# Performance work log

Measured on AMD Instinct MI355X. Metric: run time of the kernel, lower is better.

## Reference

```python
import jax, jax.numpy as jnp
import numpy as np

B, N, D, H, QK, FF, E, K = 32, 400, 128, 8, 16, 512, 8, 2
LOSS_COEF = 1e-2


def layer_norm(x, g, b, eps=1e-5):
    m = x.mean(-1, keepdims=True)
    v = ((x - m) ** 2).mean(-1, keepdims=True)
    return (x - m) / jnp.sqrt(v + eps) * g + b


def cv_sq(x, eps=1e-10):
    return x.var() / (x.mean() ** 2 + eps)


def setup_inputs() -> dict:
    key = jax.random.key(0)
    ks = jax.random.split(key, 10)
    w = lambda i, shape: jax.random.normal(ks[i], shape, jnp.float32) * 0.02
    return {
        "x": jax.random.normal(ks[0], (B, N, D), jnp.float32),
        "Wq": w(1, (D, H * QK)),
        "Wk": w(2, (D, H * QK)),
        "Wv": w(3, (D, H * QK)),
        "Wo": w(4, (H * QK, D)),
        "bo": jnp.zeros((D,), jnp.float32),
        "ln1_g": jnp.ones((D,), jnp.float32),
        "ln1_b": jnp.zeros((D,), jnp.float32),
        "w_gate": w(5, (D, E)),
        "W1": w(6, (E, D, FF)),
        "b1": jnp.zeros((E, FF), jnp.float32),
        "W2": w(7, (E, FF, D)),
        "b2": jnp.zeros((E, D), jnp.float32),
        "ln2_g": jnp.ones((D,), jnp.float32),
        "ln2_b": jnp.zeros((D,), jnp.float32),
    }


def reference(x, Wq, Wk, Wv, Wo, bo, ln1_g, ln1_b, w_gate, W1, b1, W2, b2, ln2_g, ln2_b):
    b, n, d = x.shape
    # multi-head self-attention (no mask in encoder)
    q = (x @ Wq).reshape(b, n, H, QK).transpose(0, 2, 1, 3)  # [b,h,n,qk]
    k = (x @ Wk).reshape(b, n, H, QK).transpose(0, 2, 1, 3)
    v = (x @ Wv).reshape(b, n, H, QK).transpose(0, 2, 1, 3)
    score = jnp.einsum("bhnd,bhmd->bhnm", q, k) / (QK ** 0.5)
    weights = jax.nn.softmax(score, axis=-1)
    out = jnp.einsum("bhnm,bhmd->bhnd", weights, v)
    out_concat = out.transpose(0, 2, 1, 3).reshape(b, n, H * QK)
    mh = out_concat @ Wo + bo
    out1 = layer_norm(x + mh, ln1_g, ln1_b)

    # MoE feed-forward: noisy top-k gating in eval mode (clean logits)
    xf = out1.reshape(-1, d)                       # [T, D]
    T = xf.shape[0]
    logits = xf @ w_gate                           # [T, E]
    top_vals, top_idx = jax.lax.top_k(logits, K)   # [T, K]
    top_gates = jax.nn.softmax(top_vals, axis=-1)
    gates = jnp.zeros((T, E), xf.dtype).at[jnp.arange(T)[:, None], top_idx].set(top_gates)
    # dense per-expert compute, sparse combine (same math as dispatch/combine)
    h = jax.nn.relu(jnp.einsum("td,edf->etf", xf, W1) + b1[:, None, :])  # [E,T,FF]
    y = jnp.einsum("etf,efd->etd", h, W2) + b2[:, None, :]               # [E,T,D]
    moe_out = jnp.einsum("etd,te->td", y, gates).reshape(b, n, d)
    importance = gates.sum(0)
    load = (gates > 0).sum(0).astype(xf.dtype)
    moe_loss = (cv_sq(importance) + cv_sq(load)) * LOSS_COEF

    out3 = layer_norm(out1 + moe_out, ln2_g, ln2_b)
    return (out3, moe_loss)
```

## Files before the change

### kernel.cpp

```cpp
#include <hip/hip_runtime.h>
#include <hip/hip_bf16.h>
#include <math.h>

#define Bb 32
#define Nn 400
#define Dd 128
#define Hh 8
#define QKd 16
#define FFd 512
#define Ee 8
#define Tt (Bb*Nn)
#define KPAD 434
#define PP2 34

typedef __attribute__((ext_vector_type(8))) __bf16 bf16x8;
typedef __attribute__((ext_vector_type(4))) float f32x4;

#if defined(__has_builtin)
#if __has_builtin(__builtin_amdgcn_exp2f)
#define EXP2(x) __builtin_amdgcn_exp2f(x)
#endif
#endif
#ifndef EXP2
#define EXP2(x) __expf((x) * 0.69314718f)
#endif

__device__ __forceinline__ unsigned short f2bfu(float f){
  union { __hip_bfloat16 h; unsigned short u; } v;
  v.h = __float2bfloat16(f);
  return v.u;
}
__device__ __forceinline__ short f2bf(float f){ return (short)f2bfu(f); }
__device__ __forceinline__ unsigned pack2bf(float a, float b){
  return (unsigned)f2bfu(a) | ((unsigned)f2bfu(b) << 16);
}
__device__ __forceinline__ bf16x8 zero_bf16x8(){
  union { uint4 u; bf16x8 b; } z;
  z.u.x = 0u; z.u.y = 0u; z.u.z = 0u; z.u.w = 0u;
  return z.b;
}

__global__ __launch_bounds__(256) void prep_kernel(
    const float* __restrict__ W1, const float* __restrict__ W2, const float* __restrict__ Wo,
    const float* __restrict__ Wq, const float* __restrict__ Wk, const float* __restrict__ Wv,
    short* __restrict__ W1t, short* __restrict__ W2t, short* __restrict__ wo_t,
    short* __restrict__ qkvw, int* __restrict__ gmeta)
{
  const int bid = blockIdx.x;
  if (bid == 0 && threadIdx.x < 24) gmeta[threadIdx.x] = 0;

  const float* in; short* out; int C, tile;
  if (bid < 512)        { int e = bid >> 6;         tile = bid & 63;          in = W1 + e*65536; out = W1t + e*65536; C = 512; }
  else if (bid < 1024)  { int e = (bid - 512) >> 6; tile = (bid - 512) & 63;  in = W2 + e*65536; out = W2t + e*65536; C = 128; }
  else if (bid < 1040)  { tile = bid - 1024; in = Wo; out = wo_t;          C = 128; }
  else if (bid < 1056)  { tile = bid - 1040; in = Wq; out = qkvw;          C = 128; }
  else if (bid < 1072)  { tile = bid - 1056; in = Wk; out = qkvw + 16384;  C = 128; }
  else                  { tile = bid - 1072; in = Wv; out = qkvw + 32768;  C = 128; }
  const int R = (bid < 512) ? 128 : (bid < 1024 ? 512 : 128);

  __shared__ float t32[32][33];
  const int nCt = C >> 5;
  const int c0 = (tile % nCt) << 5;
  const int r0 = (tile / nCt) << 5;
  const int tx = threadIdx.x & 31, ty = threadIdx.x >> 5;
  #pragma unroll
  for (int i = 0; i < 4; ++i)
    t32[ty + 8*i][tx] = in[(size_t)(r0 + ty + 8*i) * C + c0 + tx];
  __syncthreads();
  #pragma unroll
  for (int i = 0; i < 4; ++i)
    out[(size_t)(c0 + ty + 8*i) * R + r0 + tx] = f2bf(t32[tx][ty + 8*i]);
}

__global__ __launch_bounds__(512) void qkv_kernel(const float* __restrict__ x,
    const short* __restrict__ qkvw,
    short* __restrict__ q, short* __restrict__ k, short* __restrict__ v)
{
  __shared__ short xsh[64][136];
  __shared__ short xsl[64][136];
  const int tid = threadIdx.x;
  const int t0 = blockIdx.x * 64;

  #pragma unroll
  for (int it = 0; it < 4; ++it) {
    int lin = it * 512 + tid;
    int r = lin >> 5;
    int c4 = (lin & 31) << 2;
    float4 xv = *(const float4*)&x[(size_t)(t0 + r) * Dd + c4];
    unsigned h01 = pack2bf(xv.x, xv.y);
    unsigned h23 = pack2bf(xv.z, xv.w);
    union { unsigned u; float f; } ua, ub, uc, ud;
    ua.u = h01 << 16; ub.u = h01 & 0xFFFF0000u;
    uc.u = h23 << 16; ud.u = h23 & 0xFFFF0000u;
    unsigned l01 = pack2bf(xv.x - ua.f, xv.y - ub.f);
    unsigned l23 = pack2bf(xv.z - uc.f, xv.w - ud.f);
    uint2 ph; ph.x = h01; ph.y = h23;
    uint2 pl; pl.x = l01; pl.y = l23;
    *(uint2*)&xsh[r][c4] = ph;
    *(uint2*)&xsl[r][c4] = pl;
  }
  __syncthreads();

  const int lane = tid & 63, w = tid >> 6;
  const int l15 = lane & 15, l4 = lane >> 4;

  f32x4 zero4 = {0.f, 0.f, 0.f, 0.f};
  f32x4 acc[3][4];
  #pragma unroll
  for (int ot = 0; ot < 3; ++ot)
    #pragma unroll
    for (int mt = 0; mt < 4; ++mt) acc[ot][mt] = zero4;

  #pragma unroll
  for (int kt = 0; kt < 4; ++kt) {
    bf16x8 bmh[4], bml[4];
    #pragma unroll
    for (int mt = 0; mt < 4; ++mt) {
      bmh[mt] = *(const bf16x8*)&xsh[mt*16 + l15][kt*32 + l4*8];
      bml[mt] = *(const bf16x8*)&xsl[mt*16 + l15][kt*32 + l4*8];
    }
    #pragma unroll
    for (int ot = 0; ot < 3; ++ot) {
      bf16x8 a = *(const bf16x8*)&qkvw[(size_t)(w*48 + ot*16 + l15) * Dd + kt*32 + l4*8];
      #pragma unroll
      for (int mt = 0; mt < 4; ++mt) {
        acc[ot][mt] = __builtin_amdgcn_mfma_f32_16x16x32_bf16(a, bmh[mt], acc[ot][mt], 0, 0, 0);
        acc[ot][mt] = __builtin_amdgcn_mfma_f32_16x16x32_bf16(a, bml[mt], acc[ot][mt], 0, 0, 0);
      }
    }
  }

  #pragma unroll
  for (int ot = 0; ot < 3; ++ot) {
    const int ob = w*48 + ot*16;
    const int sel = ob >> 7;
    const int hz = (ob & 127) >> 4;
    #pragma unroll
    for (int mt = 0; mt < 4; ++mt) {
      int t = t0 + mt*16 + l15;
      int b = t / Nn, n = t - b * Nn;
      size_t bhn = (size_t)(b*Hh + hz) * Nn + n;
      f32x4 a = acc[ot][mt];
      uint2 p;
      if (sel == 0) {
        p.x = pack2bf(a[0]*0.36067376f, a[1]*0.36067376f);
        p.y = pack2bf(a[2]*0.36067376f, a[3]*0.36067376f);
        *(uint2*)&q[bhn*16 + l4*4] = p;
      } else if (sel == 1) {
        p.x = pack2bf(a[0], a[1]);
        p.y = pack2bf(a[2], a[3]);
        *(uint2*)&k[bhn*16 + l4*4] = p;
      } else {
        p.x = pack2bf(a[0], a[1]);
        p.y = pack2bf(a[2], a[3]);
        *(uint2*)&v[bhn*16 + l4*4] = p;
      }
    }
  }
}

__global__ __launch_bounds__(1024) void attn_kernel(const short* __restrict__ q,
    const short* __restrict__ k, const short* __restrict__ v, short* __restrict__ attn_b)
{
  __shared__ short VT[16 * KPAD];
  __shared__ short P[16][4][16 * PP2];
  const int tid = threadIdx.x;
  const int bh = blockIdx.x;

  {
    const unsigned* vg = (const unsigned*)(v + (size_t)bh * 400 * 16);
    #pragma unroll
    for (int it = 0; it < 4; ++it) {
      int lin = it*1024 + tid;
      if (lin < 3200) {
        int key = lin >> 3, dp = lin & 7;
        unsigned pv = vg[key*8 + dp];
        VT[(2*dp)  * KPAD + key] = (short)(pv & 0xffffu);
        VT[(2*dp+1)* KPAD + key] = (short)(pv >> 16);
      }
    }
    if (tid < 256) {
      int d = tid >> 4, key = 400 + (tid & 15);
      VT[d*KPAD + key] = 0;
    }
  }
  __syncthreads();

  const int w = tid >> 6, lane = tid & 63;
  const int l15 = lane & 15, g = lane >> 4;
  const int p = w & 7, hh = w >> 3;
  const int cc0 = hh ? 7 : 0;
  const int cc1 = hh ? 13 : 7;

  f32x4 zero4 = {0.f, 0.f, 0.f, 0.f};
  f32x4 o[4];
  float lsum[4];
  bf16x8 qf[4];
  #pragma unroll
  for (int i = 0; i < 4; ++i) {
    o[i] = zero4; lsum[i] = 0.f;
    int qt = p + 8*i;
    if (qt < 25 && g < 2)
      qf[i] = *(const bf16x8*)&q[((size_t)bh*400 + qt*16 + l15)*16 + 8*g];
    else
      qf[i] = zero_bf16x8();
  }

  for (int cc = cc0; cc < cc1; ++cc) {
    #pragma unroll
    for (int sub = 0; sub < 2; ++sub) {
      const int kt = cc*2 + sub;
      if (kt < 25) {
        bf16x8 kf;
        if (g < 2) kf = *(const bf16x8*)&k[((size_t)bh*400 + kt*16 + l15)*16 + 8*g];
        else       kf = zero_bf16x8();
        #pragma unroll
        for (int i = 0; i < 4; ++i) {
          int qt = p + 8*i;
          if (qt < 25) {
            f32x4 s = __builtin_amdgcn_mfma_f32_16x16x32_bf16(kf, qf[i], zero4, 0, 0, 0);
            float p0 = EXP2(s[0]);
            float p1 = EXP2(s[1]);
            float p2 = EXP2(s[2]);
            float p3 = EXP2(s[3]);
            lsum[i] += (p0 + p1) + (p2 + p3);
            uint2 pk;
            pk.x = pack2bf(p0, p1);
            pk.y = pack2bf(p2, p3);
            *(uint2*)&P[w][i][l15*PP2 + sub*16 + 4*g] = pk;
          }
        }
      } else {
        uint2 z; z.x = 0u; z.y = 0u;
        #pragma unroll
        for (int i = 0; i < 4; ++i) {
          int qt = p + 8*i;
          if (qt < 25) *(uint2*)&P[w][i][l15*PP2 + sub*16 + 4*g] = z;
        }
      }
    }
    bf16x8 vf = *(const bf16x8*)&VT[l15*KPAD + cc*32 + 8*g];
    #pragma unroll
    for (int i = 0; i < 4; ++i) {
      int qt = p + 8*i;
      if (qt < 25) {
        bf16x8 pf = *(const bf16x8*)&P[w][i][l15*PP2 + 8*g];
        o[i] = __builtin_amdgcn_mfma_f32_16x16x32_bf16(vf, pf, o[i], 0, 0, 0);
      }
    }
  }

  #pragma unroll
  for (int i = 0; i < 4; ++i) {
    lsum[i] += __shfl_xor(lsum[i], 16, 64);
    lsum[i] += __shfl_xor(lsum[i], 32, 64);
  }

  __syncthreads();
  float* CB = (float*)&P[0][0][0];
  if (hh == 1) {
    #pragma unroll
    for (int i = 0; i < 4; ++i) {
      int qt = p + 8*i;
      if (qt < 25) {
        int base = (((p*4) + i)*64 + lane)*5;
        CB[base+0] = o[i][0]; CB[base+1] = o[i][1];
        CB[base+2] = o[i][2]; CB[base+3] = o[i][3];
        CB[base+4] = lsum[i];
      }
    }
  }
  __syncthreads();
  if (hh == 0) {
    const int b = bh >> 3, h = bh & 7;
    #pragma unroll
    for (int i = 0; i < 4; ++i) {
      int qt = p + 8*i;
      if (qt < 25) {
        int base = (((p*4) + i)*64 + lane)*5;
        float o0 = o[i][0] + CB[base+0];
        float o1 = o[i][1] + CB[base+1];
        float o2 = o[i][2] + CB[base+2];
        float o3 = o[i][3] + CB[base+3];
        float ls = lsum[i] + CB[base+4];
        float inv = 1.f / ls;
        uint2 pk;
        pk.x = pack2bf(o0*inv, o1*inv);
        pk.y = pack2bf(o2*inv, o3*inv);
        *(uint2*)&attn_b[((size_t)b*Nn + qt*16 + l15)*Dd + h*16 + 4*g] = pk;
      }
    }
  }
}

__global__ __launch_bounds__(256) void proj_ln1_gate_kernel(
    const float* __restrict__ x, const short* __restrict__ attn_b,
    const short* __restrict__ wo_t, const float* __restrict__ bo,
    const float* __restrict__ g1, const float* __restrict__ b1n,
    const float* __restrict__ w_gate,
    short* __restrict__ out1b,
    int* __restrict__ cnt, float* __restrict__ imp, float* __restrict__ loadv,
    int* __restrict__ etok, float* __restrict__ egate)
{
  __shared__ short as_[64][136];
  __shared__ float reds[4][64];
  __shared__ float reds2[4][64];
  __shared__ float mv[64][2];
  __shared__ float lgs[64*8];
  __shared__ float wgs[128*8];
  __shared__ float s_imp[8], s_load[8];
  __shared__ int s_cnt[8], s_base[8];

  const int tid = threadIdx.x;
  const int t0 = blockIdx.x * 64;

  #pragma unroll
  for (int it = 0; it < 8; ++it) {
    int lin = it * 256 + tid;
    int r = lin >> 5;
    int c4 = (lin & 31) << 2;
    *(uint2*)&as_[r][c4] = *(const uint2*)&attn_b[(size_t)(t0 + r) * Dd + c4];
  }
  #pragma unroll
  for (int it = 0; it < 4; ++it) wgs[it*256 + tid] = w_gate[it*256 + tid];
  lgs[tid] = 0.f; lgs[tid + 256] = 0.f;
  if (tid < 8) { s_imp[tid] = 0.f; s_load[tid] = 0.f; s_cnt[tid] = 0; }
  __syncthreads();

  const int lane = tid & 63, w = tid >> 6;
  const int l15 = lane & 15, l4 = lane >> 4;

  f32x4 zero4 = {0.f, 0.f, 0.f, 0.f};
  f32x4 y[2][4];
  #pragma unroll
  for (int dt = 0; dt < 2; ++dt)
    #pragma unroll
    for (int mt = 0; mt < 4; ++mt) y[dt][mt] = zero4;

  #pragma unroll
  for (int kt = 0; kt < 4; ++kt) {
    bf16x8 a0 = *(const bf16x8*)&wo_t[(size_t)(w*32 + l15) * Dd + kt*32 + l4*8];
    bf16x8 a1 = *(const bf16x8*)&wo_t[(size_t)(w*32 + 16 + l15) * Dd + kt*32 + l4*8];
    bf16x8 bm[4];
    #pragma unroll
    for (int mt = 0; mt < 4; ++mt)
      bm[mt] = *(const bf16x8*)&as_[mt*16 + l15][kt*32 + l4*8];
    #pragma unroll
    for (int mt = 0; mt < 4; ++mt) {
      y[0][mt] = __builtin_amdgcn_mfma_f32_16x16x32_bf16(a0, bm[mt], y[0][mt], 0, 0, 0);
      y[1][mt] = __builtin_amdgcn_mfma_f32_16x16x32_bf16(a1, bm[mt], y[1][mt], 0, 0, 0);
    }
  }

  float4 bov[2];
  bov[0] = *(const float4*)&bo[w*32 + 0*16 + l4*4];
  bov[1] = *(const float4*)&bo[w*32 + 1*16 + l4*4];
  float sP[4], s2P[4];
  #pragma unroll
  for (int mt = 0; mt < 4; ++mt) { sP[mt] = 0.f; s2P[mt] = 0.f; }
  #pragma unroll
  for (int mt = 0; mt < 4; ++mt) {
    int row = mt*16 + l15;
    #pragma unroll
    for (int dt = 0; dt < 2; ++dt) {
      int dim = w*32 + dt*16 + l4*4;
      float4 xv = *(const float4*)&x[(size_t)(t0 + row) * Dd + dim];
      float4 bv = bov[dt];
      f32x4 r = y[dt][mt];
      r[0] += bv.x + xv.x; r[1] += bv.y + xv.y;
      r[2] += bv.z + xv.z; r[3] += bv.w + xv.w;
      y[dt][mt] = r;
      sP[mt]  += (r[0] + r[1]) + (r[2] + r[3]);
      s2P[mt] += (r[0]*r[0] + r[1]*r[1]) + (r[2]*r[2] + r[3]*r[3]);
    }
  }
  #pragma unroll
  for (int mt = 0; mt < 4; ++mt) {
    sP[mt]  += __shfl_xor(sP[mt], 16, 64);  sP[mt]  += __shfl_xor(sP[mt], 32, 64);
    s2P[mt] += __shfl_xor(s2P[mt], 16, 64); s2P[mt] += __shfl_xor(s2P[mt], 32, 64);
  }
  if (l4 == 0) {
    #pragma unroll
    for (int mt = 0; mt < 4; ++mt) {
      reds[w][mt*16 + l15] = sP[mt];
      reds2[w][mt*16 + l15] = s2P[mt];
    }
  }
  __syncthreads();
  if (tid < 64) {
    float s = reds[0][tid] + reds[1][tid] + reds[2][tid] + reds[3][tid];
    float s2 = reds2[0][tid] + reds2[1][tid] + reds2[2][tid] + reds2[3][tid];
    float m = s * (1.f/128.f);
    float var = s2 * (1.f/128.f) - m*m;
    mv[tid][0] = m;
    mv[tid][1] = rsqrtf(var + 1e-5f);
  }
  __syncthreads();

  float4 gv[2], bv2[2];
  #pragma unroll
  for (int dt = 0; dt < 2; ++dt) {
    gv[dt]  = *(const float4*)&g1[w*32 + dt*16 + l4*4];
    bv2[dt] = *(const float4*)&b1n[w*32 + dt*16 + l4*4];
  }
  #pragma unroll
  for (int mt = 0; mt < 4; ++mt) {
    int row = mt*16 + l15;
    float m = mv[row][0], inv = mv[row][1];
    float lg[8];
    #pragma unroll
    for (int e = 0; e < 8; ++e) lg[e] = 0.f;
    #pragma unroll
    for (int dt = 0; dt < 2; ++dt) {
      int dim = w*32 + dt*16 + l4*4;
      f32x4 r = y[dt][mt];
      float o0 = (r[0]-m)*inv*((float*)&gv[dt])[0] + ((float*)&bv2[dt])[0];
      float o1 = (r[1]-m)*inv*((float*)&gv[dt])[1] + ((float*)&bv2[dt])[1];
      float o2 = (r[2]-m)*inv*((float*)&gv[dt])[2] + ((float*)&bv2[dt])[2];
      float o3 = (r[3]-m)*inv*((float*)&gv[dt])[3] + ((float*)&bv2[dt])[3];
      uint2 p; p.x = pack2bf(o0, o1); p.y = pack2bf(o2, o3);
      *(uint2*)&out1b[(size_t)(t0 + row) * Dd + dim] = p;
      #pragma unroll
      for (int e = 0; e < 8; ++e)
        lg[e] += o0*wgs[(dim+0)*8+e] + o1*wgs[(dim+1)*8+e]
               + o2*wgs[(dim+2)*8+e] + o3*wgs[(dim+3)*8+e];
    }
    #pragma unroll
    for (int e = 0; e < 8; ++e) {
      lg[e] += __shfl_xor(lg[e], 16, 64);
      lg[e] += __shfl_xor(lg[e], 32, 64);
    }
    if (l4 == 0) {
      #pragma unroll
      for (int e = 0; e < 8; ++e) atomicAdd(&lgs[row*8 + e], lg[e]);
    }
  }
  __syncthreads();

  int i0 = 0, i1 = -1, p0 = 0, p1 = 0;
  float g0 = 0.f, gg1 = 0.f;
  if (tid < 64) {
    float lgv[8];
    #pragma unroll
    for (int e = 0; e < 8; ++e) lgv[e] = lgs[tid*8 + e];
    float v0 = lgv[0];
    #pragma unroll
    for (int e = 1; e < 8; ++e) if (lgv[e] > v0) { v0 = lgv[e]; i0 = e; }
    float v1 = -INFINITY;
    #pragma unroll
    for (int e = 0; e < 8; ++e) if (e != i0 && lgv[e] > v1) { v1 = lgv[e]; i1 = e; }
    g0 = 1.f / (1.f + __expf(v1 - v0));
    gg1 = 1.f - g0;
    atomicAdd(&s_imp[i0], g0);  atomicAdd(&s_imp[i1], gg1);
    atomicAdd(&s_load[i0], 1.f); atomicAdd(&s_load[i1], 1.f);
    p0 = atomicAdd(&s_cnt[i0], 1);
    p1 = atomicAdd(&s_cnt[i1], 1);
  }
  __syncthreads();
  if (tid < 8) {
    s_base[tid] = atomicAdd(&cnt[tid], s_cnt[tid]);
    atomicAdd(&imp[tid], s_imp[tid]);
    atomicAdd(&loadv[tid], s_load[tid]);
  }
  __syncthreads();
  if (tid < 64) {
    int t = t0 + tid;
    int o0 = i0 * Tt + s_base[i0] + p0;
    etok[o0] = t;               egate[o0] = g0;
    int o1 = i1 * Tt + s_base[i1] + p1;
    etok[o1] = t | (1 << 30);   egate[o1] = gg1;
  }
}

union MoeShared {
  struct { short xs[64][136]; short hs[2][64][136]; } s;
  float comb[4][64][36];
};

__global__ __launch_bounds__(512) void moe_kernel(const short* __restrict__ out1b,
    const short* __restrict__ W1t, const float* __restrict__ b1,
    const short* __restrict__ W2t, const float* __restrict__ b2,
    const int* __restrict__ cnt, const int* __restrict__ etok, const float* __restrict__ egate,
    short* __restrict__ moe0, short* __restrict__ moe1)
{
  __shared__ MoeShared su;
  __shared__ int els[64];
  __shared__ float gls[64];

  const int e = blockIdx.y;
  const int count = cnt[e];
  const int t0 = blockIdx.x * 64;
  if (t0 >= count) return;
  const int nt = min(64, count - t0);
  const int tid = threadIdx.x;

  if (tid < 64) {
    int idx = (tid < nt) ? tid : 0;
    els[tid] = etok[e * Tt + t0 + idx];
    gls[tid] = (tid < nt) ? egate[e * Tt + t0 + tid] : 0.f;
  }
  __syncthreads();

  #pragma unroll
  for (int it = 0; it < 4; ++it) {
    int lin = it * 512 + tid;
    int r = lin >> 5;
    int c4 = (lin & 31) << 2;
    int tok = els[r] & 0x3FFFFFFF;
    *(uint2*)&su.s.xs[r][c4] = *(const uint2*)&out1b[(size_t)tok * Dd + c4];
  }
  __syncthreads();

  const int lane = tid & 63;
  const int w = tid >> 6;
  const int grp = w >> 2;
  const int wp = w & 3;
  const int l15 = lane & 15;
  const int l4 = lane >> 4;

  f32x4 zero4 = {0.f, 0.f, 0.f, 0.f};
  f32x4 y[2][4];
  #pragma unroll
  for (int dt = 0; dt < 2; ++dt)
    #pragma unroll
    for (int mt = 0; mt < 4; ++mt) y[dt][mt] = zero4;

  const short* W1p = W1t + (size_t)e * FFd * Dd;
  const short* W2p = W2t + (size_t)e * Dd * FFd;
  short (*hsg)[136] = su.s.hs[grp];

  #pragma unroll
  for (int c = 0; c < 2; ++c) {
    const int ch = grp*2 + c;
    f32x4 h[2][4];
    #pragma unroll
    for (int ft = 0; ft < 2; ++ft)
      #pragma unroll
      for (int mt = 0; mt < 4; ++mt) h[ft][mt] = zero4;

    #pragma unroll
    for (int kt = 0; kt < 4; ++kt) {
      bf16x8 a0 = *(const bf16x8*)&W1p[(size_t)(ch*128 + wp*32 + 0*16 + l15) * Dd + kt*32 + l4*8];
      bf16x8 a1 = *(const bf16x8*)&W1p[(size_t)(ch*128 + wp*32 + 1*16 + l15) * Dd + kt*32 + l4*8];
      bf16x8 bm[4];
      #pragma unroll
      for (int mt = 0; mt < 4; ++mt)
        bm[mt] = *(const bf16x8*)&su.s.xs[mt*16 + l15][kt*32 + l4*8];
      #pragma unroll
      for (int mt = 0; mt < 4; ++mt) {
        h[0][mt] = __builtin_amdgcn_mfma_f32_16x16x32_bf16(a0, bm[mt], h[0][mt], 0, 0, 0);
        h[1][mt] = __builtin_amdgcn_mfma_f32_16x16x32_bf16(a1, bm[mt], h[1][mt], 0, 0, 0);
      }
    }

    float4 b1v0 = *(const float4*)&b1[e*FFd + ch*128 + wp*32 + 0*16 + l4*4];
    float4 b1v1 = *(const float4*)&b1[e*FFd + ch*128 + wp*32 + 1*16 + l4*4];
    __syncthreads();
    #pragma unroll
    for (int mt = 0; mt < 4; ++mt) {
      uint2 p0, p1;
      p0.x = pack2bf(fmaxf(h[0][mt][0] + b1v0.x, 0.f), fmaxf(h[0][mt][1] + b1v0.y, 0.f));
      p0.y = pack2bf(fmaxf(h[0][mt][2] + b1v0.z, 0.f), fmaxf(h[0][mt][3] + b1v0.w, 0.f));
      *(uint2*)&hsg[mt*16 + l15][wp*32 + 0*16 + l4*4] = p0;
      p1.x = pack2bf(fmaxf(h[1][mt][0] + b1v1.x, 0.f), fmaxf(h[1][mt][1] + b1v1.y, 0.f));
      p1.y = pack2bf(fmaxf(h[1][mt][2] + b1v1.z, 0.f), fmaxf(h[1][mt][3] + b1v1.w, 0.f));
      *(uint2*)&hsg[mt*16 + l15][wp*32 + 1*16 + l4*4] = p1;
    }
    __syncthreads();

    #pragma unroll
    for (int kt = 0; kt < 4; ++kt) {
      bf16x8 a0 = *(const bf16x8*)&W2p[(size_t)(wp*32 + 0*16 + l15) * FFd + ch*128 + kt*32 + l4*8];
      bf16x8 a1 = *(const bf16x8*)&W2p[(size_t)(wp*32 + 1*16 + l15) * FFd + ch*128 + kt*32 + l4*8];
      bf16x8 bm[4];
      #pragma unroll
      for (int mt = 0; mt < 4; ++mt)
        bm[mt] = *(const bf16x8*)&hsg[mt*16 + l15][kt*32 + l4*8];
      #pragma unroll
      for (int mt = 0; mt < 4; ++mt) {
        y[0][mt] = __builtin_amdgcn_mfma_f32_16x16x32_bf16(a0, bm[mt], y[0][mt], 0, 0, 0);
        y[1][mt] = __builtin_amdgcn_mfma_f32_16x16x32_bf16(a1, bm[mt], y[1][mt], 0, 0, 0);
      }
    }
  }

  __syncthreads();
  if (grp == 1) {
    float* cb = &su.comb[wp][lane][0];
    #pragma unroll
    for (int dt = 0; dt < 2; ++dt)
      #pragma unroll
      for (int mt = 0; mt < 4; ++mt) {
        float4 v4;
        v4.x = y[dt][mt][0]; v4.y = y[dt][mt][1];
        v4.z = y[dt][mt][2]; v4.w = y[dt][mt][3];
        *(float4*)&cb[(dt*4+mt)*4] = v4;
      }
  }
  __syncthreads();
  if (grp == 0) {
    const float* cb = &su.comb[wp][lane][0];
    float4 b2v[2];
    b2v[0] = *(const float4*)&b2[e*Dd + wp*32 + 0*16 + l4*4];
    b2v[1] = *(const float4*)&b2[e*Dd + wp*32 + 1*16 + l4*4];
    #pragma unroll
    for (int mt = 0; mt < 4; ++mt) {
      int m = mt*16 + l15;
      if (m < nt) {
        int raw = els[m];
        int t = raw & 0x3FFFFFFF;
        float g = gls[m];
        short* basep = (raw & (1 << 30)) ? moe1 : moe0;
        #pragma unroll
        for (int dt = 0; dt < 2; ++dt) {
          float4 yo = *(const float4*)&cb[(dt*4+mt)*4];
          float v0 = g * (y[dt][mt][0] + yo.x + ((dt == 0) ? b2v[0].x : b2v[1].x));
          float v1 = g * (y[dt][mt][1] + yo.y + ((dt == 0) ? b2v[0].y : b2v[1].y));
          float v2 = g * (y[dt][mt][2] + yo.z + ((dt == 0) ? b2v[0].z : b2v[1].z));
          float v3 = g * (y[dt][mt][3] + yo.w + ((dt == 0) ? b2v[0].w : b2v[1].w));
          uint2 p; p.x = pack2bf(v0, v1); p.y = pack2bf(v2, v3);
          *(uint2*)&basep[(size_t)t * Dd + wp*32 + dt*16 + l4*4] = p;
        }
      }
    }
  }
}

__global__ __launch_bounds__(256) void ln2_kernel(const short* __restrict__ out1b,
    const short* __restrict__ moe0, const short* __restrict__ moe1,
    const float* __restrict__ g, const float* __restrict__ bb,
    const float* __restrict__ imp, const float* __restrict__ loadv,
    float* __restrict__ out, float* __restrict__ out_loss)
{
  const int tid = threadIdx.x;
  const int lane = tid & 63;
  const int t = blockIdx.x * 4 + (tid >> 6);
  const int j = lane * 2;

  unsigned xo = *(const unsigned*)&out1b[(size_t)t * Dd + j];
  unsigned m0 = *(const unsigned*)&moe0[(size_t)t * Dd + j];
  unsigned m1 = *(const unsigned*)&moe1[(size_t)t * Dd + j];
  union { unsigned u; float f; } xa, xb, a, b, c, d;
  xa.u = xo << 16; xb.u = xo & 0xFFFF0000u;
  a.u = m0 << 16; b.u = m0 & 0xFFFF0000u;
  c.u = m1 << 16; d.u = m1 & 0xFFFF0000u;
  float r0 = xa.f + a.f + c.f;
  float r1 = xb.f + b.f + d.f;

  float s = r0 + r1;
  float s2 = r0*r0 + r1*r1;
  #pragma unroll
  for (int off = 32; off > 0; off >>= 1) {
    s  += __shfl_xor(s, off, 64);
    s2 += __shfl_xor(s2, off, 64);
  }
  float mean = s * (1.f/128.f);
  float var = s2 * (1.f/128.f) - mean*mean;
  float inv = rsqrtf(var + 1e-5f);
  float2 ov;
  ov.x = (r0 - mean) * inv * g[j]   + bb[j];
  ov.y = (r1 - mean) * inv * g[j+1] + bb[j+1];
  *(float2*)&out[(size_t)t * Dd + j] = ov;

  if (blockIdx.x == 0 && tid == 0) {
    float m1s = 0.f;
    for (int e = 0; e < 8; ++e) m1s += imp[e];
    m1s *= 0.125f;
    float v1 = 0.f;
    for (int e = 0; e < 8; ++e) { float dd = imp[e] - m1s; v1 += dd * dd; }
    v1 *= 0.125f;
    float c1 = v1 / (m1s * m1s + 1e-10f);
    float m2 = 0.f;
    for (int e = 0; e < 8; ++e) m2 += loadv[e];
    m2 *= 0.125f;
    float v2 = 0.f;
    for (int e = 0; e < 8; ++e) { float dd = loadv[e] - m2; v2 += dd * dd; }
    v2 *= 0.125f;
    float c2 = v2 / (m2 * m2 + 1e-10f);
    out_loss[0] = (c1 + c2) * 0.01f;
  }
}

extern "C" void kernel_launch(void* const* d_in, const int* in_sizes, int n_in,
                              void* d_out, int out_size, void* d_ws, size_t ws_size,
                              hipStream_t stream)
{
  (void)in_sizes; (void)n_in; (void)out_size; (void)ws_size;
  const float* x      = (const float*)d_in[0];
  const float* Wq     = (const float*)d_in[1];
  const float* Wk     = (const float*)d_in[2];
  const float* Wv     = (const float*)d_in[3];
  const float* Wo     = (const float*)d_in[4];
  const float* bo     = (const float*)d_in[5];
  const float* ln1_g  = (const float*)d_in[6];
  const float* ln1_b  = (const float*)d_in[7];
  const float* w_gate = (const float*)d_in[8];
  const float* W1     = (const float*)d_in[9];
  const float* b1     = (const float*)d_in[10];
  const float* W2     = (const float*)d_in[11];
  const float* b2     = (const float*)d_in[12];
  const float* ln2_g  = (const float*)d_in[13];
  const float* ln2_b  = (const float*)d_in[14];

  char* wsb = (char*)d_ws;
  size_t off = 0;
  short* attn_b  = (short*)(wsb + off); off += (size_t)Tt*Dd*2;
  short* out1b   = (short*)(wsb + off); off += (size_t)Tt*Dd*2;
  short* moe0    = (short*)(wsb + off); off += (size_t)Tt*Dd*2;
  short* moe1    = (short*)(wsb + off); off += (size_t)Tt*Dd*2;
  short* q_bf    = (short*)(wsb + off); off += (size_t)256*400*16*2;
  short* k_bf    = (short*)(wsb + off); off += (size_t)256*400*16*2;
  short* v_bf    = (short*)(wsb + off); off += (size_t)256*400*16*2;
  short* W1t     = (short*)(wsb + off); off += (size_t)Ee*FFd*Dd*2;
  short* W2t     = (short*)(wsb + off); off += (size_t)Ee*FFd*Dd*2;
  short* wo_t    = (short*)(wsb + off); off += (size_t)Dd*Dd*2;
  short* qkvw    = (short*)(wsb + off); off += (size_t)384*Dd*2;
  int*   gmeta   = (int*)(wsb + off);   off += 256;
  int*   etok    = (int*)(wsb + off);   off += (size_t)Ee*Tt*4;
  float* egate   = (float*)(wsb + off); off += (size_t)Ee*Tt*4;

  int*   cnt   = gmeta;
  float* imp   = (float*)(gmeta + 8);
  float* loadv = (float*)(gmeta + 16);

  float* out3 = (float*)d_out;
  float* loss = out3 + Tt * Dd;

  prep_kernel<<<1088, 256, 0, stream>>>(W1, W2, Wo, Wq, Wk, Wv, W1t, W2t, wo_t, qkvw, gmeta);
  qkv_kernel<<<200, 512, 0, stream>>>(x, qkvw, q_bf, k_bf, v_bf);
  attn_kernel<<<256, 1024, 0, stream>>>(q_bf, k_bf, v_bf, attn_b);
  proj_ln1_gate_kernel<<<200, 256, 0, stream>>>(x, attn_b, wo_t, bo, ln1_g, ln1_b, w_gate,
                                                out1b, cnt, imp, loadv, etok, egate);
  moe_kernel<<<dim3(200, 8), 512, 0, stream>>>(out1b, W1t, b1, W2t, b2, cnt, etok, egate, moe0, moe1);
  ln2_kernel<<<3200, 256, 0, stream>>>(out1b, moe0, moe1, ln2_g, ln2_b, imp, loadv, out3, loss);
}
```

Measured before the change: 78.49 us.

## Split output projection K-dimension across two wave groups in proj_ln1_gate kernel

```diff
diff --git a/kernel.cpp b/kernel.cpp
--- a/kernel.cpp
+++ b/kernel.cpp
@@ -293,7 +293,12 @@
   }
 }
 
-__global__ __launch_bounds__(256) void proj_ln1_gate_kernel(
+union ProjShared {
+  short as_[64][136];
+  float comb[4][64][36];
+};
+
+__global__ __launch_bounds__(512) void proj_ln1_gate_kernel(
     const float* __restrict__ x, const short* __restrict__ attn_b,
     const short* __restrict__ wo_t, const float* __restrict__ bo,
     const float* __restrict__ g1, const float* __restrict__ b1n,
@@ -302,7 +307,7 @@
     int* __restrict__ cnt, float* __restrict__ imp, float* __restrict__ loadv,
     int* __restrict__ etok, float* __restrict__ egate)
 {
-  __shared__ short as_[64][136];
+  __shared__ ProjShared su;
   __shared__ float reds[4][64];
   __shared__ float reds2[4][64];
   __shared__ float mv[64][2];
@@ -315,19 +320,20 @@
   const int t0 = blockIdx.x * 64;
 
   #pragma unroll
-  for (int it = 0; it < 8; ++it) {
-    int lin = it * 256 + tid;
+  for (int it = 0; it < 4; ++it) {
+    int lin = it * 512 + tid;
     int r = lin >> 5;
     int c4 = (lin & 31) << 2;
-    *(uint2*)&as_[r][c4] = *(const uint2*)&attn_b[(size_t)(t0 + r) * Dd + c4];
-  }
-  #pragma unroll
-  for (int it = 0; it < 4; ++it) wgs[it*256 + tid] = w_gate[it*256 + tid];
-  lgs[tid] = 0.f; lgs[tid + 256] = 0.f;
+    *(uint2*)&su.as_[r][c4] = *(const uint2*)&attn_b[(size_t)(t0 + r) * Dd + c4];
+  }
+  #pragma unroll
+  for (int it = 0; it < 2; ++it) wgs[it*512 + tid] = w_gate[it*512 + tid];
+  lgs[tid] = 0.f;
   if (tid < 8) { s_imp[tid] = 0.f; s_load[tid] = 0.f; s_cnt[tid] = 0; }
   __syncthreads();
 
   const int lane = tid & 63, w = tid >> 6;
+  const int wp = w & 3, grp = w >> 2;
   const int l15 = lane & 15, l4 = lane >> 4;
 
   f32x4 zero4 = {0.f, 0.f, 0.f, 0.f};
@@ -338,13 +344,14 @@
     for (int mt = 0; mt < 4; ++mt) y[dt][mt] = zero4;
 
   #pragma unroll
-  for (int kt = 0; kt < 4; ++kt) {
-    bf16x8 a0 = *(const bf16x8*)&wo_t[(size_t)(w*32 + l15) * Dd + kt*32 + l4*8];
-    bf16x8 a1 = *(const bf16x8*)&wo_t[(size_t)(w*32 + 16 + l15) * Dd + kt*32 + l4*8];
+  for (int kk = 0; kk < 2; ++kk) {
+    const int kt = grp*2 + kk;
+    bf16x8 a0 = *(const bf16x8*)&wo_t[(size_t)(wp*32 + l15) * Dd + kt*32 + l4*8];
+    bf16x8 a1 = *(const bf16x8*)&wo_t[(size_t)(wp*32 + 16 + l15) * Dd + kt*32 + l4*8];
     bf16x8 bm[4];
     #pragma unroll
     for (int mt = 0; mt < 4; ++mt)
-      bm[mt] = *(const bf16x8*)&as_[mt*16 + l15][kt*32 + l4*8];
+      bm[mt] = *(const bf16x8*)&su.as_[mt*16 + l15][kt*32 + l4*8];
     #pragma unroll
     for (int mt = 0; mt < 4; ++mt) {
       y[0][mt] = __builtin_amdgcn_mfma_f32_16x16x32_bf16(a0, bm[mt], y[0][mt], 0, 0, 0);
@@ -352,38 +359,56 @@
     }
   }
 
-  float4 bov[2];
-  bov[0] = *(const float4*)&bo[w*32 + 0*16 + l4*4];
-  bov[1] = *(const float4*)&bo[w*32 + 1*16 + l4*4];
+  __syncthreads();
+  if (grp == 1) {
+    float* cb = &su.comb[wp][lane][0];
+    #pragma unroll
+    for (int dt = 0; dt < 2; ++dt)
+      #pragma unroll
+      for (int mt = 0; mt < 4; ++mt) {
+        float4 v4;
+        v4.x = y[dt][mt][0]; v4.y = y[dt][mt][1];
+        v4.z = y[dt][mt][2]; v4.w = y[dt][mt][3];
+        *(float4*)&cb[(dt*4+mt)*4] = v4;
+      }
+  }
+  __syncthreads();
+
   float sP[4], s2P[4];
-  #pragma unroll
-  for (int mt = 0; mt < 4; ++mt) { sP[mt] = 0.f; s2P[mt] = 0.f; }
-  #pragma unroll
-  for (int mt = 0; mt < 4; ++mt) {
-    int row = mt*16 + l15;
-    #pragma unroll
-    for (int dt = 0; dt < 2; ++dt) {
-      int dim = w*32 + dt*16 + l4*4;
-      float4 xv = *(const float4*)&x[(size_t)(t0 + row) * Dd + dim];
-      float4 bv = bov[dt];
-      f32x4 r = y[dt][mt];
-      r[0] += bv.x + xv.x; r[1] += bv.y + xv.y;
-      r[2] += bv.z + xv.z; r[3] += bv.w + xv.w;
-      y[dt][mt] = r;
-      sP[mt]  += (r[0] + r[1]) + (r[2] + r[3]);
-      s2P[mt] += (r[0]*r[0] + r[1]*r[1]) + (r[2]*r[2] + r[3]*r[3]);
-    }
-  }
-  #pragma unroll
-  for (int mt = 0; mt < 4; ++mt) {
-    sP[mt]  += __shfl_xor(sP[mt], 16, 64);  sP[mt]  += __shfl_xor(sP[mt], 32, 64);
-    s2P[mt] += __shfl_xor(s2P[mt], 16, 64); s2P[mt] += __shfl_xor(s2P[mt], 32, 64);
-  }
-  if (l4 == 0) {
+  if (grp == 0) {
+    const float* cb = &su.comb[wp][lane][0];
+    float4 bov[2];
+    bov[0] = *(const float4*)&bo[wp*32 + 0*16 + l4*4];
+    bov[1] = *(const float4*)&bo[wp*32 + 1*16 + l4*4];
     #pragma unroll
     for (int mt = 0; mt < 4; ++mt) {
-      reds[w][mt*16 + l15] = sP[mt];
-      reds2[w][mt*16 + l15] = s2P[mt];
+      int row = mt*16 + l15;
+      sP[mt] = 0.f; s2P[mt] = 0.f;
+      #pragma unroll
+      for (int dt = 0; dt < 2; ++dt) {
+        int dim = wp*32 + dt*16 + l4*4;
+        float4 xv = *(const float4*)&x[(size_t)(t0 + row) * Dd + dim];
+        float4 yo = *(const float4*)&cb[(dt*4+mt)*4];
+        float4 bv = bov[dt];
+        f32x4 r = y[dt][mt];
+        r[0] += yo.x + bv.x + xv.x; r[1] += yo.y + bv.y + xv.y;
+        r[2] += yo.z + bv.z + xv.z; r[3] += yo.w + bv.w + xv.w;
+        y[dt][mt] = r;
+        sP[mt]  += (r[0] + r[1]) + (r[2] + r[3]);
+        s2P[mt] += (r[0]*r[0] + r[1]*r[1]) + (r[2]*r[2] + r[3]*r[3]);
+      }
+    }
+    #pragma unroll
+    for (int mt = 0; mt < 4; ++mt) {
+      sP[mt]  += __shfl_xor(sP[mt], 16, 64);  sP[mt]  += __shfl_xor(sP[mt], 32, 64);
+      s2P[mt] += __shfl_xor(s2P[mt], 16, 64); s2P[mt] += __shfl_xor(s2P[mt], 32, 64);
+    }
+    if (l4 == 0) {
+      #pragma unroll
+      for (int mt = 0; mt < 4; ++mt) {
+        reds[wp][mt*16 + l15] = sP[mt];
+        reds2[wp][mt*16 + l15] = s2P[mt];
+      }
     }
   }
   __syncthreads();
@@ -397,42 +422,44 @@
   }
   __syncthreads();
 
-  float4 gv[2], bv2[2];
-  #pragma unroll
-  for (int dt = 0; dt < 2; ++dt) {
-    gv[dt]  = *(const float4*)&g1[w*32 + dt*16 + l4*4];
-    bv2[dt] = *(const float4*)&b1n[w*32 + dt*16 + l4*4];
-  }
-  #pragma unroll
-  for (int mt = 0; mt < 4; ++mt) {
-    int row = mt*16 + l15;
-    float m = mv[row][0], inv = mv[row][1];
-    float lg[8];
-    #pragma unroll
-    for (int e = 0; e < 8; ++e) lg[e] = 0.f;
+  if (grp == 0) {
+    float4 gv[2], bv2[2];
     #pragma unroll
     for (int dt = 0; dt < 2; ++dt) {
-      int dim = w*32 + dt*16 + l4*4;
-      f32x4 r = y[dt][mt];
-      float o0 = (r[0]-m)*inv*((float*)&gv[dt])[0] + ((float*)&bv2[dt])[0];
-      float o1 = (r[1]-m)*inv*((float*)&gv[dt])[1] + ((float*)&bv2[dt])[1];
-      float o2 = (r[2]-m)*inv*((float*)&gv[dt])[2] + ((float*)&bv2[dt])[2];
-      float o3 = (r[3]-m)*inv*((float*)&gv[dt])[3] + ((float*)&bv2[dt])[3];
-      uint2 p; p.x = pack2bf(o0, o1); p.y = pack2bf(o2, o3);
-      *(uint2*)&out1b[(size_t)(t0 + row) * Dd + dim] = p;
-      #pragma unroll
-      for (int e = 0; e < 8; ++e)
-        lg[e] += o0*wgs[(dim+0)*8+e] + o1*wgs[(dim+1)*8+e]
-               + o2*wgs[(dim+2)*8+e] + o3*wgs[(dim+3)*8+e];
-    }
-    #pragma unroll
-    for (int e = 0; e < 8; ++e) {
-      lg[e] += __shfl_xor(lg[e], 16, 64);
-      lg[e] += __shfl_xor(lg[e], 32, 64);
-    }
-    if (l4 == 0) {
-      #pragma unroll
-      for (int e = 0; e < 8; ++e) atomicAdd(&lgs[row*8 + e], lg[e]);
+      gv[dt]  = *(const float4*)&g1[wp*32 + dt*16 + l4*4];
+      bv2[dt] = *(const float4*)&b1n[wp*32 + dt*16 + l4*4];
+    }
+    #pragma unroll
+    for (int mt = 0; mt < 4; ++mt) {
+      int row = mt*16 + l15;
+      float m = mv[row][0], inv = mv[row][1];
+      float lg[8];
+      #pragma unroll
+      for (int e = 0; e < 8; ++e) lg[e] = 0.f;
+      #pragma unroll
+      for (int dt = 0; dt < 2; ++dt) {
+        int dim = wp*32 + dt*16 + l4*4;
+        f32x4 r = y[dt][mt];
+        float o0 = (r[0]-m)*inv*((float*)&gv[dt])[0] + ((float*)&bv2[dt])[0];
+        float o1 = (r[1]-m)*inv*((float*)&gv[dt])[1] + ((float*)&bv2[dt])[1];
+        float o2 = (r[2]-m)*inv*((float*)&gv[dt])[2] + ((float*)&bv2[dt])[2];
+        float o3 = (r[3]-m)*inv*((float*)&gv[dt])[3] + ((float*)&bv2[dt])[3];
+        uint2 p; p.x = pack2bf(o0, o1); p.y = pack2bf(o2, o3);
+        *(uint2*)&out1b[(size_t)(t0 + row) * Dd + dim] = p;
+        #pragma unroll
+        for (int e = 0; e < 8; ++e)
+          lg[e] += o0*wgs[(dim+0)*8+e] + o1*wgs[(dim+1)*8+e]
+                 + o2*wgs[(dim+2)*8+e] + o3*wgs[(dim+3)*8+e];
+      }
+      #pragma unroll
+      for (int e = 0; e < 8; ++e) {
+        lg[e] += __shfl_xor(lg[e], 16, 64);
+        lg[e] += __shfl_xor(lg[e], 32, 64);
+      }
+      if (l4 == 0) {
+        #pragma unroll
+        for (int e = 0; e < 8; ++e) atomicAdd(&lgs[row*8 + e], lg[e]);
+      }
     }
   }
   __syncthreads();
@@ -729,7 +756,7 @@
   prep_kernel<<<1088, 256, 0, stream>>>(W1, W2, Wo, Wq, Wk, Wv, W1t, W2t, wo_t, qkvw, gmeta);
   qkv_kernel<<<200, 512, 0, stream>>>(x, qkvw, q_bf, k_bf, v_bf);
   attn_kernel<<<256, 1024, 0, stream>>>(q_bf, k_bf, v_bf, attn_b);
-  proj_ln1_gate_kernel<<<200, 256, 0, stream>>>(x, attn_b, wo_t, bo, ln1_g, ln1_b, w_gate,
+  proj_ln1_gate_kernel<<<200, 512, 0, stream>>>(x, attn_b, wo_t, bo, ln1_g, ln1_b, w_gate,
                                                 out1b, cnt, imp, loadv, etok, egate);
   moe_kernel<<<dim3(200, 8), 512, 0, stream>>>(out1b, W1t, b1, W2t, b2, cnt, etok, egate, moe0, moe1);
   ln2_kernel<<<3200, 256, 0, stream>>>(out1b, moe0, moe1, ln2_g, ln2_b, imp, loadv, out3, loss);
```

New measurement: 79.06 us. No clear change (+0.7%).
